# Kernel optimization log

Measured on AMD Instinct MI355X. Metric: run time of the kernel, lower is better.

## Reference

```python
import jax, jax.numpy as jnp
import numpy as np

NP_, NA_, NS_ = 4096, 4096, 1
E_ = 131072
DIN, DOUT, H = 256, 64, 4
SLOPE = 0.2  # leaky relu negative slope


def _leaky(x):
    return jnp.where(x >= 0, x, SLOPE * x)


def setup_inputs() -> dict:
    key = jax.random.key(0)
    ks = iter(jax.random.split(key, 64))
    inp = {}
    inp['feat_P'] = jax.random.normal(next(ks), (NP_, DIN), jnp.float32)
    inp['feat_A'] = jax.random.normal(next(ks), (NA_, DIN), jnp.float32)
    inp['feat_state'] = jax.random.normal(next(ks), (NS_, DIN), jnp.float32)
    for name in ['P', 'A', 'p2p', 'p2a', 'a2p', 'a2a', 'p2s', 'a2s', 'in']:
        inp['W_' + name] = jax.random.normal(next(ks), (DOUT * H, DIN), jnp.float32) / np.sqrt(DIN)
        inp['b_' + name] = jax.random.normal(next(ks), (DOUT * H,), jnp.float32) * 0.01
    for name in ['p2p', 'p2a', 'a2p', 'a2a', 'p2s', 'a2s']:
        inp['att_%s_src' % name] = jax.random.normal(next(ks), (1, H, DOUT), jnp.float32) * 0.1
        inp['att_%s_dst' % name] = jax.random.normal(next(ks), (1, H, DOUT), jnp.float32) * 0.1
    for name, ns, nd in [('p2p', NP_, NP_), ('p2a', NP_, NA_), ('a2p', NA_, NP_), ('a2a', NA_, NA_)]:
        inp['e_%s_src' % name] = jax.random.randint(next(ks), (E_,), 0, ns, jnp.int32)
        inp['e_%s_dst' % name] = jax.random.randint(next(ks), (E_,), 0, nd, jnp.int32)
    inp['e_p2s_src'] = jnp.arange(NP_, dtype=jnp.int32)
    inp['e_p2s_dst'] = jnp.zeros((NP_,), jnp.int32)
    inp['e_a2s_src'] = jnp.arange(NA_, dtype=jnp.int32)
    inp['e_a2s_dst'] = jnp.zeros((NA_,), jnp.int32)
    return inp


def _msg_agg(feat_src, W, b, att_s, att_d, Wh_dst, src, dst, n_dst):
    # per-edge lossy_u_mul_e with comm_loss == 0 (noise branch dead):
    # gather src features, per-edge linear, per-edge softmax over HEADS (torch Softmax(dim=1)).
    h = feat_src[src]                                    # [E, DIN]
    Wh = (h @ W.T + b).reshape(-1, H, DOUT)              # [E, H, D]
    a_s = jnp.sum(Wh * att_s, axis=-1, keepdims=True)    # [E, H, 1]
    a_d = jnp.sum(Wh_dst[dst] * att_d, axis=-1, keepdims=True)
    attn = jax.nn.softmax(_leaky(a_s + a_d), axis=1)     # softmax over heads, as in original
    return jax.ops.segment_sum(Wh * attn, dst, num_segments=n_dst)


def _edge_softmax_agg(Wh_src, att_s, Wh_state, att_d, src, dst, n_dst):
    # dgl edge_softmax: destination-grouped stable softmax over incoming edges.
    a_s = jnp.sum(Wh_src * att_s, axis=-1, keepdims=True)[src]    # [E, H, 1]
    a_d = jnp.sum(Wh_state * att_d, axis=-1, keepdims=True)[dst]  # [E, H, 1]
    e = _leaky(a_s + a_d)
    m = jax.ops.segment_max(e, dst, num_segments=n_dst)
    ex = jnp.exp(e - m[dst])
    den = jax.ops.segment_sum(ex, dst, num_segments=n_dst)
    a = ex / den[dst]
    return jax.ops.segment_sum(Wh_src[src] * a, dst, num_segments=n_dst)


def reference(feat_P, feat_A, feat_state,
              W_P, b_P, W_A, b_A, W_p2p, b_p2p, W_p2a, b_p2a, W_a2p, b_a2p,
              W_a2a, b_a2a, W_p2s, b_p2s, W_a2s, b_a2s, W_in, b_in,
              att_p2p_src, att_p2p_dst, att_p2a_src, att_p2a_dst,
              att_a2p_src, att_a2p_dst, att_a2a_src, att_a2a_dst,
              att_p2s_src, att_p2s_dst, att_a2s_src, att_a2s_dst,
              e_p2p_src, e_p2p_dst, e_p2a_src, e_p2a_dst,
              e_a2p_src, e_a2p_dst, e_a2a_src, e_a2a_dst,
              e_p2s_src, e_p2s_dst, e_a2s_src, e_a2s_dst):
    Whp = (feat_P @ W_P.T + b_P).reshape(NP_, H, DOUT)
    Wha = (feat_A @ W_A.T + b_A).reshape(NA_, H, DOUT)
    Whp2s = (feat_P @ W_p2s.T + b_p2s).reshape(NP_, H, DOUT)
    Wha2s = (feat_A @ W_a2s.T + b_a2s).reshape(NA_, H, DOUT)
    Whin = (feat_state @ W_in.T + b_in).reshape(NS_, H, DOUT)

    ft_p2p = _msg_agg(feat_P, W_p2p, b_p2p, att_p2p_src, att_p2p_dst, Whp, e_p2p_src, e_p2p_dst, NP_)
    ft_p2a = _msg_agg(feat_P, W_p2a, b_p2a, att_p2a_src, att_p2a_dst, Wha, e_p2a_src, e_p2a_dst, NA_)
    ft_a2p = _msg_agg(feat_A, W_a2p, b_a2p, att_a2p_src, att_a2p_dst, Whp, e_a2p_src, e_a2p_dst, NP_)
    ft_a2a = _msg_agg(feat_A, W_a2a, b_a2a, att_a2a_src, att_a2a_dst, Wha, e_a2a_src, e_a2a_dst, NA_)

    ft_p2s = _edge_softmax_agg(Whp2s, att_p2s_src, Whin, att_p2s_dst, e_p2s_src, e_p2s_dst, NS_)
    ft_a2s = _edge_softmax_agg(Wha2s, att_a2s_src, Whin, att_a2s_dst, e_a2s_src, e_a2s_dst, NS_)

    h_P = jax.nn.relu(Whp + ft_p2p + ft_a2p)
    h_A = jax.nn.relu(Wha + ft_p2a + ft_a2a)
    h_S = jax.nn.relu(Whin + ft_p2s + ft_a2s)
    return (h_P, h_A, h_S)
```

## Files before the change

kernel.cpp:

```cpp
#include <hip/hip_runtime.h>

#define NPA   4096
#define DHD   256
#define EDG   131072
#define OS    4104
#define PST   64
#define NCH   32
#define TBL_SZ ((size_t)NPA * DHD)

#define B_AH    ((size_t)0)
#define B_WH    (B_AH + 2 * TBL_SZ * 2)
#define B_TBL   (B_WH + (size_t)8 * 65536 * 2)
#define B_SCORE (B_TBL + 8 * TBL_SZ * 2)
#define B_CNTP  (B_SCORE + (size_t)10 * NPA * 4 * 4)
#define B_CBASE (B_CNTP + (size_t)4 * NCH * NPA * 4)
#define B_OFFS  (B_CBASE + (size_t)4 * NCH * NPA * 4)
#define B_PKT   (B_OFFS + (size_t)4 * OS * 4)
#define B_WHIN  (B_PKT + (size_t)4 * EDG * 16)
#define B_SCD   (B_WHIN + 256 * 4)
#define B_NUMP  (B_SCD + 8 * 4)
#define B_DENP  (B_NUMP + (size_t)2 * PST * 256 * 4)

typedef _Float16 half8 __attribute__((ext_vector_type(8)));
typedef _Float16 half4 __attribute__((ext_vector_type(4)));
typedef _Float16 half2v __attribute__((ext_vector_type(2)));
typedef float floatx4 __attribute__((ext_vector_type(4)));

struct CastArgs { const float* src[10]; };
struct GemmArgs {
    const float* b[8];
    const float* att0[8]; const float* att1[8];
    int sj0[8]; int sj1[8];
};
struct EdgeArgs { const int* src[4]; const int* dst[4]; };

__device__ __forceinline__ float lrelu(float x) { return x >= 0.0f ? x : 0.2f * x; }

__device__ __forceinline__ int pack2(float a, float b) {
    half2v h = {(_Float16)a, (_Float16)b};
    return __builtin_bit_cast(int, h);
}
__device__ __forceinline__ half2v bc2(int v) { return __builtin_bit_cast(half2v, v); }

__device__ __forceinline__ half2v asplat(const int4& p, int head) {
    int w = (head & 2) ? p.z : p.y;
    int b = (head & 1) ? ((w >> 16) & 0xffff) : (w & 0xffff);
    return bc2(b | (b << 16));
}

__global__ __launch_bounds__(256) void prep_kernel(CastArgs ca, EdgeArgs ea,
        const float* __restrict__ fs, const float* __restrict__ Win,
        const float* __restrict__ bin, const float* __restrict__ attP,
        const float* __restrict__ attA, _Float16* __restrict__ dst,
        int* __restrict__ cntp, float* __restrict__ whin, float* __restrict__ scd) {
    __shared__ int hist[NPA];
    int bid = blockIdx.x;
    int tid = threadIdx.x;
    if (bid < 128) {
        int r = bid >> 5;
        int c = bid & 31;
        const int* dp = ea.dst[r] + c * 4096;
#pragma unroll
        for (int i = 0; i < 16; ++i) hist[tid + i * 256] = 0;
        __syncthreads();
#pragma unroll
        for (int k = 0; k < 16; ++k)
            atomicAdd(&hist[dp[k * 256 + tid]], 1);
        __syncthreads();
        int* cr = cntp + (size_t)bid * NPA;
#pragma unroll
        for (int i = 0; i < 16; ++i)
            cr[tid + i * 256] = hist[tid + i * 256];
        return;
    }
    if (bid == 128) {
        float* sf = (float*)hist;
        sf[tid] = fs[tid];
        __syncthreads();
        const float* wr = Win + (size_t)tid * 256;
        float acc = bin[tid];
        for (int k = 0; k < 256; k += 4) {
            float4 wv = *(const float4*)(wr + k);
            acc += wv.x * sf[k] + wv.y * sf[k + 1] + wv.z * sf[k + 2] + wv.w * sf[k + 3];
        }
        whin[tid] = acc;
        float v1 = acc * attP[tid];
        float v2 = acc * attA[tid];
        for (int d = 32; d; d >>= 1) { v1 += __shfl_xor(v1, d); v2 += __shfl_xor(v2, d); }
        if ((tid & 63) == 0) { scd[tid >> 6] = v1; scd[4 + (tid >> 6)] = v2; }
        return;
    }
    size_t i4 = ((size_t)(bid - 129) * 256 + tid) * 4;
    const float* s; size_t off;
    if (i4 < TBL_SZ)            { s = ca.src[0]; off = i4; }
    else if (i4 < 2 * TBL_SZ)   { s = ca.src[1]; off = i4 - TBL_SZ; }
    else { size_t r = i4 - 2 * TBL_SZ; s = ca.src[2 + (r >> 16)]; off = r & 65535; }
    float4 v = *(const float4*)(s + off);
    half4 hh = {(_Float16)v.x, (_Float16)v.y, (_Float16)v.z, (_Float16)v.w};
    *(half4*)(dst + i4) = hh;
}

__global__ __launch_bounds__(256) void gemm_scan(const _Float16* __restrict__ Ah,
        const _Float16* __restrict__ Whb, GemmArgs ga, const int* __restrict__ cntp,
        _Float16* __restrict__ tblBase, float* __restrict__ score,
        int* __restrict__ offs, int* __restrict__ cbase) {
    int bid = blockIdx.x;
    int t = threadIdx.x;
    if (bid < 64) {
        int gid = bid * 256 + t;
        int r = gid >> 12;
        int d = gid & 4095;
        const int* cp = cntp + (size_t)r * NCH * NPA + d;
        int* cb = cbase + (size_t)r * NCH * NPA + d;
        int running = 0;
#pragma unroll
        for (int c = 0; c < NCH; ++c) {
            cb[(size_t)c * NPA] = running;
            running += cp[(size_t)c * NPA];
        }
        return;
    }
    if (bid < 68) {
        int r = bid - 64;
        const int4* cpr = (const int4*)(cntp + (size_t)r * NCH * NPA);
        int4 s[4];
#pragma unroll
        for (int q = 0; q < 4; ++q) {
            int4 acc = {0, 0, 0, 0};
            for (int c = 0; c < NCH; ++c) {
                int4 u = cpr[(size_t)c * (NPA / 4) + t * 4 + q];
                acc.x += u.x; acc.y += u.y; acc.z += u.z; acc.w += u.w;
            }
            s[q] = acc;
        }
        int lsum = 0;
#pragma unroll
        for (int q = 0; q < 4; ++q) lsum += s[q].x + s[q].y + s[q].z + s[q].w;
        int wave = t >> 6, lane = t & 63;
        int sc = lsum;
#pragma unroll
        for (int d = 1; d < 64; d <<= 1) {
            int u = __shfl_up(sc, d);
            if (lane >= d) sc += u;
        }
        __shared__ int ws4[4];
        if (lane == 63) ws4[wave] = sc;
        __syncthreads();
        int wb = 0;
        for (int w = 0; w < 4; ++w) if (w < wave) wb += ws4[w];
        int run = wb + sc - lsum;
        int* of = offs + (size_t)r * OS;
#pragma unroll
        for (int q = 0; q < 4; ++q) {
            int4 o;
            o.x = run; run += s[q].x;
            o.y = run; run += s[q].y;
            o.z = run; run += s[q].z;
            o.w = run; run += s[q].w;
            ((int4*)of)[t * 4 + q] = o;
        }
        if (t == 255) of[NPA] = run;
        return;
    }
    int g = bid - 68;
    int j = g >> 6;
    int mt = g & 63;
    int w = t >> 6, lane = t & 63;
    int quad = lane >> 4, l16 = lane & 15;
    const _Float16* A = Ah + (size_t)(j >> 2) * TBL_SZ;
    const _Float16* W = Whb + (size_t)j * 65536;
    const float* bias = ga.b[j];
    _Float16* out = tblBase + (size_t)j * TBL_SZ;
    int mr0 = mt * 64;
    int nc0 = w * 64;
    const _Float16* ap[4];
    const _Float16* bp[4];
#pragma unroll
    for (int g2 = 0; g2 < 4; ++g2) {
        ap[g2] = A + (size_t)(mr0 + g2 * 16 + l16) * 256 + quad * 8;
        bp[g2] = W + (size_t)(nc0 + g2 * 16 + l16) * 256 + quad * 8;
    }
    floatx4 acc[4][4];
#pragma unroll
    for (int rg = 0; rg < 4; ++rg)
#pragma unroll
        for (int cg = 0; cg < 4; ++cg) acc[rg][cg] = (floatx4){0, 0, 0, 0};
#pragma unroll
    for (int k0 = 0; k0 < 256; k0 += 32) {
        half8 av[4], bv[4];
#pragma unroll
        for (int g2 = 0; g2 < 4; ++g2) av[g2] = *(const half8*)(ap[g2] + k0);
#pragma unroll
        for (int g2 = 0; g2 < 4; ++g2) bv[g2] = *(const half8*)(bp[g2] + k0);
#pragma unroll
        for (int rg = 0; rg < 4; ++rg)
#pragma unroll
            for (int cg = 0; cg < 4; ++cg)
                acc[rg][cg] = __builtin_amdgcn_mfma_f32_16x16x32_f16(av[rg], bv[cg], acc[rg][cg], 0, 0, 0);
    }
    float bc[4];
#pragma unroll
    for (int cg = 0; cg < 4; ++cg) bc[cg] = bias[nc0 + cg * 16 + l16];
#pragma unroll
    for (int rg = 0; rg < 4; ++rg)
#pragma unroll
        for (int i = 0; i < 4; ++i) {
            int row = mr0 + rg * 16 + quad * 4 + i;
#pragma unroll
            for (int cg = 0; cg < 4; ++cg)
                out[(size_t)row * 256 + nc0 + cg * 16 + l16] = (_Float16)(acc[rg][cg][i] + bc[cg]);
        }
#pragma unroll
    for (int tt = 0; tt < 2; ++tt) {
        const float* att = tt ? ga.att1[j] : ga.att0[j];
        int sj = tt ? ga.sj1[j] : ga.sj0[j];
        if (!att) continue;
        float at[4];
#pragma unroll
        for (int cg = 0; cg < 4; ++cg) at[cg] = att[nc0 + cg * 16 + l16];
        float* sb = score + (size_t)sj * NPA * 4;
#pragma unroll
        for (int rg = 0; rg < 4; ++rg)
#pragma unroll
            for (int i = 0; i < 4; ++i) {
                float p = (acc[rg][0][i] + bc[0]) * at[0] + (acc[rg][1][i] + bc[1]) * at[1]
                        + (acc[rg][2][i] + bc[2]) * at[2] + (acc[rg][3][i] + bc[3]) * at[3];
                p += __shfl_xor(p, 1); p += __shfl_xor(p, 2);
                p += __shfl_xor(p, 4); p += __shfl_xor(p, 8);
                if (l16 == 0) {
                    int row = mr0 + rg * 16 + quad * 4 + i;
                    sb[(size_t)row * 4 + w] = p;
                }
            }
    }
}

__global__ __launch_bounds__(256) void scatter_state(EdgeArgs ea,
        const float* __restrict__ score, const int* __restrict__ cbase,
        const int* __restrict__ offs, int4* __restrict__ pkt,
        const _Float16* __restrict__ tblBase, const float* __restrict__ scd,
        float* __restrict__ numP, float* __restrict__ denP) {
    __shared__ int lpos[NPA];
    int bid = blockIdx.x;
    int t = threadIdx.x;
    if (bid >= 128) {
        int sb = bid - 128;
        int r = sb >> 6;
        int blk = sb & 63;
        int h = t >> 6;
        const _Float16* wh = tblBase + (size_t)(r == 0 ? 3 : 7) * TBL_SZ;
        const float* as = score + (size_t)(8 + r) * NPA * 4;
        float dh = scd[r * 4 + h];
        float dsum = 0.0f, acc = 0.0f;
        for (int i = blk; i < NPA; i += PST) {
            float x = lrelu(as[(size_t)i * 4 + h] + dh);
            float w = __expf(x);
            dsum += w;
            acc += w * (float)wh[(size_t)i * 256 + t];
        }
        numP[(size_t)(r * PST + blk) * 256 + t] = acc;
        if ((t & 63) == 0) denP[(size_t)(r * PST + blk) * 4 + h] = dsum;
        return;
    }
    int r = bid >> 5;
    int c = bid & 31;
    const int* cb = cbase + (size_t)(r * NCH + c) * NPA;
    const int* of = offs + (size_t)r * OS;
#pragma unroll
    for (int i = 0; i < 16; ++i)
        lpos[t + i * 256] = cb[t + i * 256] + of[t + i * 256];
    __syncthreads();
    const int* sp = ea.src[r] + c * 4096;
    const int* dp = ea.dst[r] + c * 4096;
    const float* as = score + (size_t)r * NPA * 4;
    const float* ad = score + (size_t)(4 + r) * NPA * 4;
    int4* pkb = pkt + (size_t)r * EDG;
#pragma unroll 4
    for (int k = 0; k < 16; ++k) {
        int e = k * 256 + t;
        int s = sp[e];
        int d = dp[e];
        float4 av = *(const float4*)&as[(size_t)s * 4];
        float4 dv = *(const float4*)&ad[(size_t)d * 4];
        float x0 = lrelu(av.x + dv.x), x1 = lrelu(av.y + dv.y);
        float x2 = lrelu(av.z + dv.z), x3 = lrelu(av.w + dv.w);
        float m = fmaxf(fmaxf(x0, x1), fmaxf(x2, x3));
        float e0 = __expf(x0 - m), e1 = __expf(x1 - m), e2 = __expf(x2 - m), e3 = __expf(x3 - m);
        float inv = 1.0f / (e0 + e1 + e2 + e3);
        int pos = atomicAdd(&lpos[d], 1);
        int4 pk = {s, pack2(e0 * inv, e1 * inv), pack2(e2 * inv, e3 * inv), 0};
        pkb[pos] = pk;
    }
}

__global__ __launch_bounds__(256) void agg_final(const int* __restrict__ offs,
        const int4* __restrict__ pkt, const _Float16* __restrict__ tblBase,
        const float* __restrict__ whin, const float* __restrict__ numP,
        const float* __restrict__ denP, float* __restrict__ outBase) {
    int bid = blockIdx.x;
    int tid = threadIdx.x;
    if (bid == 2048) {
        int t = tid;
        int h = t >> 6;
        float n0 = 0.f, n1 = 0.f, d0 = 0.f, d1 = 0.f;
        for (int b = 0; b < PST; ++b) {
            n0 += numP[(size_t)b * 256 + t];
            n1 += numP[(size_t)(PST + b) * 256 + t];
            d0 += denP[(size_t)b * 4 + h];
            d1 += denP[(size_t)(PST + b) * 4 + h];
        }
        float v = whin[t] + n0 / d0 + n1 / d1;
        outBase[2 * TBL_SZ + t] = fmaxf(v, 0.f);
        return;
    }
    int side = bid >> 10;
    int bx = bid & 1023;
    int wave = tid >> 6, lane = tid & 63;
    int dn = bx * 4 + wave;
    int h = lane >> 5, l32 = lane & 31;
    int head = l32 >> 3;
    half2v acc[4] = {{0,0},{0,0},{0,0},{0,0}};
    const int srcIdx[4] = {1, 2, 5, 6};
    const int4 z = {0, 0, 0, 0};
#pragma unroll
    for (int q = 0; q < 2; ++q) {
        int r = side + q * 2;
        const int* of = offs + (size_t)r * OS;
        const int4* pkb = pkt + (size_t)r * EDG;
        const _Float16* wh = tblBase + (size_t)srcIdx[r] * TBL_SZ;
        int beg = of[dn], end = of[dn + 1];
        int i = beg;
        int4 p[8];
#pragma unroll
        for (int u = 0; u < 8; ++u)
            p[u] = (i + 2 * u + h < end) ? pkb[i + 2 * u + h] : z;
        while (i < end) {
            int ni = i + 16;
            half8 w[8];
#pragma unroll
            for (int u = 0; u < 8; ++u)
                w[u] = *(const half8*)(wh + (size_t)p[u].x * 256 + l32 * 8);
            int4 n[8];
#pragma unroll
            for (int u = 0; u < 8; ++u)
                n[u] = (ni + 2 * u + h < end) ? pkb[ni + 2 * u + h] : z;
#pragma unroll
            for (int u = 0; u < 8; ++u) {
                half2v a = asplat(p[u], head);
                int4 iw = __builtin_bit_cast(int4, w[u]);
                acc[0] += bc2(iw.x) * a; acc[1] += bc2(iw.y) * a;
                acc[2] += bc2(iw.z) * a; acc[3] += bc2(iw.w) * a;
            }
#pragma unroll
            for (int u = 0; u < 8; ++u) p[u] = n[u];
            i = ni;
        }
    }
    float f[8];
#pragma unroll
    for (int k = 0; k < 4; ++k) {
        f[2 * k] = (float)acc[k][0];
        f[2 * k + 1] = (float)acc[k][1];
    }
#pragma unroll
    for (int k = 0; k < 8; ++k) f[k] += __shfl_xor(f[k], 32);
    if (h == 0) {
        const _Float16* skip = tblBase + (size_t)(side * 4) * TBL_SZ + (size_t)dn * 256 + l32 * 8;
        half8 sv = *(const half8*)skip;
        float* op = outBase + ((size_t)side * NPA + dn) * 256 + l32 * 8;
        float4 o0 = {fmaxf(f[0] + (float)sv[0], 0.f), fmaxf(f[1] + (float)sv[1], 0.f),
                     fmaxf(f[2] + (float)sv[2], 0.f), fmaxf(f[3] + (float)sv[3], 0.f)};
        float4 o1 = {fmaxf(f[4] + (float)sv[4], 0.f), fmaxf(f[5] + (float)sv[5], 0.f),
                     fmaxf(f[6] + (float)sv[6], 0.f), fmaxf(f[7] + (float)sv[7], 0.f)};
        *(float4*)op = o0;
        *(float4*)(op + 4) = o1;
    }
}

extern "C" void kernel_launch(void* const* d_in, const int* in_sizes, int n_in,
                              void* d_out, int out_size, void* d_ws, size_t ws_size,
                              hipStream_t stream) {
    auto F = [&](int i) { return (const float*)d_in[i]; };
    char* ws = (char*)d_ws;
    _Float16* Ah  = (_Float16*)(ws + B_AH);
    _Float16* Whb = (_Float16*)(ws + B_WH);
    _Float16* tbl = (_Float16*)(ws + B_TBL);
    float* score  = (float*)(ws + B_SCORE);
    int* cntp     = (int*)(ws + B_CNTP);
    int* cbase    = (int*)(ws + B_CBASE);
    int* offs     = (int*)(ws + B_OFFS);
    int4* pkt     = (int4*)(ws + B_PKT);
    float* whin   = (float*)(ws + B_WHIN);
    float* scd    = (float*)(ws + B_SCD);
    float* numP   = (float*)(ws + B_NUMP);
    float* denP   = (float*)(ws + B_DENP);

    CastArgs ca = {{F(0), F(1), F(3), F(7), F(9), F(15), F(5), F(11), F(13), F(17)}};
    EdgeArgs ea = {{(const int*)d_in[33], (const int*)d_in[35], (const int*)d_in[37], (const int*)d_in[39]},
                   {(const int*)d_in[34], (const int*)d_in[36], (const int*)d_in[38], (const int*)d_in[40]}};

    prep_kernel<<<2689, 256, 0, stream>>>(ca, ea, F(2), F(19), F(20), F(30), F(32),
                                          Ah, cntp, whin, scd);

    GemmArgs ga;
    const int bIdx[8] = {4, 8, 10, 16, 6, 12, 14, 18};
    for (int j = 0; j < 8; ++j) ga.b[j] = F(bIdx[j]);
    const int a0Idx[8]  = {22, 21, 23, 29, 24, 25, 27, 31};
    const int sj0Arr[8] = { 4,  0,  1,  8,  5,  2,  3,  9};
    for (int j = 0; j < 8; ++j) {
        ga.att0[j] = F(a0Idx[j]); ga.sj0[j] = sj0Arr[j];
        ga.att1[j] = nullptr;     ga.sj1[j] = -1;
    }
    ga.att1[0] = F(26); ga.sj1[0] = 6;
    ga.att1[4] = F(28); ga.sj1[4] = 7;

    gemm_scan<<<68 + 512, 256, 0, stream>>>(Ah, Whb, ga, cntp, tbl, score, offs, cbase);
    scatter_state<<<128 + 2 * PST, 256, 0, stream>>>(ea, score, cbase, offs, pkt, tbl, scd, numP, denP);
    agg_final<<<2049, 256, 0, stream>>>(offs, pkt, tbl, whin, numP, denP, (float*)d_out);
}
```

Baseline: 231.2 us.

## Split aggregation relations across waves and combine partials through shared memory

```diff
diff --git a/kernel.cpp b/kernel.cpp
--- a/kernel.cpp
+++ b/kernel.cpp
@@ -299,7 +299,7 @@
         const float* __restrict__ denP, float* __restrict__ outBase) {
     int bid = blockIdx.x;
     int tid = threadIdx.x;
-    if (bid == 2048) {
+    if (bid == 4096) {
         int t = tid;
         int h = t >> 6;
         float n0 = 0.f, n1 = 0.f, d0 = 0.f, d1 = 0.f;
@@ -313,18 +313,20 @@
         outBase[2 * TBL_SZ + t] = fmaxf(v, 0.f);
         return;
     }
-    int side = bid >> 10;
-    int bx = bid & 1023;
+    __shared__ float pshare[2][2][32][9];
+    int side = bid >> 11;
+    int bx = bid & 2047;
     int wave = tid >> 6, lane = tid & 63;
-    int dn = bx * 4 + wave;
+    int node = wave >> 1;
+    int q = wave & 1;
+    int dn = bx * 2 + node;
     int h = lane >> 5, l32 = lane & 31;
     int head = l32 >> 3;
     half2v acc[4] = {{0,0},{0,0},{0,0},{0,0}};
     const int srcIdx[4] = {1, 2, 5, 6};
     const int4 z = {0, 0, 0, 0};
-#pragma unroll
-    for (int q = 0; q < 2; ++q) {
-        int r = side + q * 2;
+    int r = side + q * 2;
+    {
         const int* of = offs + (size_t)r * OS;
         const int4* pkb = pkt + (size_t)r * EDG;
         const _Float16* wh = tblBase + (size_t)srcIdx[r] * TBL_SZ;
@@ -365,13 +367,25 @@
 #pragma unroll
     for (int k = 0; k < 8; ++k) f[k] += __shfl_xor(f[k], 32);
     if (h == 0) {
-        const _Float16* skip = tblBase + (size_t)(side * 4) * TBL_SZ + (size_t)dn * 256 + l32 * 8;
+#pragma unroll
+        for (int k = 0; k < 8; ++k) pshare[node][q][l32][k] = f[k];
+    }
+    __syncthreads();
+    if (wave < 2 && lane < 32) {
+        int nd = wave;
+        int dn2 = bx * 2 + nd;
+        const _Float16* skip = tblBase + (size_t)(side * 4) * TBL_SZ + (size_t)dn2 * 256 + lane * 8;
         half8 sv = *(const half8*)skip;
-        float* op = outBase + ((size_t)side * NPA + dn) * 256 + l32 * 8;
-        float4 o0 = {fmaxf(f[0] + (float)sv[0], 0.f), fmaxf(f[1] + (float)sv[1], 0.f),
-                     fmaxf(f[2] + (float)sv[2], 0.f), fmaxf(f[3] + (float)sv[3], 0.f)};
-        float4 o1 = {fmaxf(f[4] + (float)sv[4], 0.f), fmaxf(f[5] + (float)sv[5], 0.f),
-                     fmaxf(f[6] + (float)sv[6], 0.f), fmaxf(f[7] + (float)sv[7], 0.f)};
+        float* op = outBase + ((size_t)side * NPA + dn2) * 256 + lane * 8;
+        float4 o0, o1;
+        o0.x = fmaxf(pshare[nd][0][lane][0] + pshare[nd][1][lane][0] + (float)sv[0], 0.f);
+        o0.y = fmaxf(pshare[nd][0][lane][1] + pshare[nd][1][lane][1] + (float)sv[1], 0.f);
+        o0.z = fmaxf(pshare[nd][0][lane][2] + pshare[nd][1][lane][2] + (float)sv[2], 0.f);
+        o0.w = fmaxf(pshare[nd][0][lane][3] + pshare[nd][1][lane][3] + (float)sv[3], 0.f);
+        o1.x = fmaxf(pshare[nd][0][lane][4] + pshare[nd][1][lane][4] + (float)sv[4], 0.f);
+        o1.y = fmaxf(pshare[nd][0][lane][5] + pshare[nd][1][lane][5] + (float)sv[5], 0.f);
+        o1.z = fmaxf(pshare[nd][0][lane][6] + pshare[nd][1][lane][6] + (float)sv[6], 0.f);
+        o1.w = fmaxf(pshare[nd][0][lane][7] + pshare[nd][1][lane][7] + (float)sv[7], 0.f);
         *(float4*)op = o0;
         *(float4*)(op + 4) = o1;
     }
@@ -416,5 +430,5 @@
 
     gemm_scan<<<68 + 512, 256, 0, stream>>>(Ah, Whb, ga, cntp, tbl, score, offs, cbase);
     scatter_state<<<128 + 2 * PST, 256, 0, stream>>>(ea, score, cbase, offs, pkt, tbl, scd, numP, denP);
-    agg_final<<<2049, 256, 0, stream>>>(offs, pkt, tbl, whin, numP, denP, (float*)d_out);
-}
+    agg_final<<<4097, 256, 0, stream>>>(offs, pkt, tbl, whin, numP, denP, (float*)d_out);
+}
```

After: 237.4 us. +2.7%, slower.
